# Kernel tuning notes

Measured on AMD Instinct MI355X. Metric: run time of the kernel, lower is better.

The kernel has to match this reference:

```python
import jax, jax.numpy as jnp
import numpy as np
from functools import partial

BLUR_K = 5
SIGMA = 1.5
DOWN = 4
SCALE = 5.0
OFFSET = 0.2

_DN = ('NCHW', 'OIHW', 'NCHW')


def _gaussian_kernel(k, sigma):
    x = jnp.arange(k, dtype=jnp.float32) - (k - 1) / 2.0
    g = jnp.exp(-x ** 2 / (2.0 * sigma ** 2))
    g2 = jnp.outer(g, g)
    g2 = g2 / g2.sum()
    return g2.reshape(1, 1, k, k)


def setup_inputs() -> dict:
    key = jax.random.key(0)
    left_rgb = jax.random.uniform(key, (16, 3, 544, 960), dtype=jnp.float32)
    return {"left_rgb": left_rgb}


def reference(left_rgb):
    B, C, H, W = left_rgb.shape
    # rgb -> gray (1x1 conv with fixed weights)
    w = jnp.array([0.2989, 0.587, 0.114], dtype=left_rgb.dtype)
    gray = jnp.einsum('bchw,c->bhw', left_rgb, w)[:, None]  # [B,1,H,W]

    # gaussian blur with reflect padding (torch F.pad mode='reflect')
    pad = BLUR_K // 2
    gray_p = jnp.pad(gray, ((0, 0), (0, 0), (pad, pad), (pad, pad)), mode='reflect')
    gk = _gaussian_kernel(BLUR_K, SIGMA).astype(left_rgb.dtype)
    gray_smooth = jax.lax.conv_general_dilated(gray_p, gk, (1, 1), 'VALID',
                                               dimension_numbers=_DN)

    # sobel gradients (cross-correlation, zero padding=1, same as torch conv2d)
    sx = jnp.array([[-1., 0., 1.], [-2., 0., 2.], [-1., 0., 1.]],
                   dtype=left_rgb.dtype).reshape(1, 1, 3, 3)
    sy = jnp.array([[-1., -2., -1.], [0., 0., 0.], [1., 2., 1.]],
                   dtype=left_rgb.dtype).reshape(1, 1, 3, 3)
    gx = jax.lax.conv_general_dilated(gray_smooth, sx, (1, 1), [(1, 1), (1, 1)],
                                      dimension_numbers=_DN)
    gy = jax.lax.conv_general_dilated(gray_smooth, sy, (1, 1), [(1, 1), (1, 1)],
                                      dimension_numbers=_DN)
    mag = jnp.sqrt(gx ** 2 + gy ** 2 + 1e-6)  # [B,1,H,W]

    # avg_pool2d kernel=stride=DOWN (H, W divisible by DOWN)
    down = mag.reshape(B, 1, H // DOWN, DOWN, W // DOWN, DOWN).mean(axis=(3, 5))

    edge_mask = jax.nn.sigmoid(SCALE * (down - OFFSET)) ** 2.0
    return edge_mask
```

## Files before the change

kernel.cpp:

```cpp
#include <hip/hip_runtime.h>
#include <cmath>

constexpr int B = 16, C = 3, H = 544, W = 960;
constexpr int OH = 136, OW = 240;
constexpr size_t HW = (size_t)H * W;

constexpr int TOH = 8, TOW = 30, NTH = 17, NTW = 8, MH = 32, MW = 120;
constexpr int TR = 40;
constexpr int TS = 132;
constexpr int TC4 = 32;
constexpr int NT = 5;

__global__ __launch_bounds__(256)
void edge_fused(const float* __restrict__ in, float* __restrict__ out,
                float gn0, float gn1, float gn2)
{
    __shared__ float tmp[TR * TS];

    const int tid = threadIdx.x;
    const int blk = blockIdx.x;
    const int tw = blk % NTW;
    const int th = (blk / NTW) % NTH;
    const int b  = blk / (NTW * NTH);
    const int mh0 = th * MH, mw0 = tw * MW;
    const float* inb = in + (size_t)b * C * HW;

    float4 Aq[NT][3], Bq[NT][3];
    float  Sc[NT][3];
    #pragma unroll
    for (int k = 0; k < NT; ++k) {
        const int idx = tid + 256 * k;
        const int r = idx >> 5;
        const int c = idx & 31;
        int g = mh0 - 4 + r;
        g = g < 0 ? -g : (g >= H ? 2 * H - 2 - g : g);
        int gcb = mw0 - 4 + 4 * c;
        gcb = gcb < 0 ? 0 : (gcb > W - 12 ? W - 12 : gcb);
        const float* p = inb + (size_t)g * W + gcb;
        #pragma unroll
        for (int ch = 0; ch < 3; ++ch) {
            Aq[k][ch] = *reinterpret_cast<const float4*>(p);
            Bq[k][ch] = *reinterpret_cast<const float4*>(p + 4);
            Sc[k][ch] = p[8];
            p += HW;
        }
    }
    #pragma unroll
    for (int k = 0; k < NT; ++k) {
        const int idx = tid + 256 * k;
        const int r = idx >> 5;
        const int c = idx & 31;
        const float a0[8] = {Aq[k][0].y, Aq[k][0].z, Aq[k][0].w, Bq[k][0].x,
                             Bq[k][0].y, Bq[k][0].z, Bq[k][0].w, Sc[k][0]};
        const float a1[8] = {Aq[k][1].y, Aq[k][1].z, Aq[k][1].w, Bq[k][1].x,
                             Bq[k][1].y, Bq[k][1].z, Bq[k][1].w, Sc[k][1]};
        const float a2[8] = {Aq[k][2].y, Aq[k][2].z, Aq[k][2].w, Bq[k][2].x,
                             Bq[k][2].y, Bq[k][2].z, Bq[k][2].w, Sc[k][2]};
        float g8[8];
        #pragma unroll
        for (int m = 0; m < 8; ++m)
            g8[m] = fmaf(0.2989f, a0[m], fmaf(0.587f, a1[m], 0.114f * a2[m]));
        float4 t;
        t.x = gn0 * g8[0] + gn1 * g8[1] + gn2 * g8[2] + gn1 * g8[3] + gn0 * g8[4];
        t.y = gn0 * g8[1] + gn1 * g8[2] + gn2 * g8[3] + gn1 * g8[4] + gn0 * g8[5];
        t.z = gn0 * g8[2] + gn1 * g8[3] + gn2 * g8[4] + gn1 * g8[5] + gn0 * g8[6];
        t.w = gn0 * g8[3] + gn1 * g8[4] + gn2 * g8[5] + gn1 * g8[6] + gn0 * g8[7];
        *reinterpret_cast<float4*>(&tmp[r * TS + 4 * c]) = t;
    }
    __syncthreads();

    if (tw == 0 || tw == NTW - 1) {
        const int ntask = (tw == 0) ? TR : 2 * TR;
        if (tid < ntask) {
            int r, c;
            if (tw == 0) { r = tid; c = 0; }
            else         { r = tid >> 1; c = 29 + (tid & 1); }
            int g = mh0 - 4 + r;
            g = g < 0 ? -g : (g >= H ? 2 * H - 2 - g : g);
            const int gcb = mw0 - 4 + 4 * c;
            float g8[8];
            #pragma unroll
            for (int m = 0; m < 8; ++m) {
                int gc = gcb + 1 + m;
                gc = gc < 0 ? -gc : (gc >= W ? 2 * W - 2 - gc : gc);
                const float* p = inb + (size_t)g * W + gc;
                g8[m] = 0.2989f * p[0] + 0.587f * p[HW] + 0.114f * p[2 * HW];
            }
            float4 t;
            t.x = gn0 * g8[0] + gn1 * g8[1] + gn2 * g8[2] + gn1 * g8[3] + gn0 * g8[4];
            t.y = gn0 * g8[1] + gn1 * g8[2] + gn2 * g8[3] + gn1 * g8[4] + gn0 * g8[5];
            t.z = gn0 * g8[2] + gn1 * g8[3] + gn2 * g8[4] + gn1 * g8[5] + gn0 * g8[6];
            t.w = gn0 * g8[3] + gn1 * g8[4] + gn2 * g8[5] + gn1 * g8[6] + gn0 * g8[7];
            *reinterpret_cast<float4*>(&tmp[r * TS + 4 * c]) = t;
        }
    }
    __syncthreads();

    if (tid < TOH * TOW) {
        const int orow = tid / TOW;
        const int ocol = tid - orow * TOW;
        const int sr0 = orow * 4, tc0 = ocol * 4;

        float sm[6][6];
        #pragma unroll
        for (int i = 0; i < 6; ++i)
            #pragma unroll
            for (int j = 0; j < 6; ++j) sm[i][j] = 0.f;

        const float gk[5] = {gn0, gn1, gn2, gn1, gn0};
        #pragma unroll
        for (int tr = 0; tr < 10; ++tr) {
            const float* p = &tmp[(sr0 + 1 + tr) * TS + tc0];
            const float4 u  = *reinterpret_cast<const float4*>(p);
            const float4 vv = *reinterpret_cast<const float4*>(p + 4);
            const float t6[6] = {u.x, u.y, u.z, u.w, vv.x, vv.y};
            #pragma unroll
            for (int i = 0; i < 6; ++i) {
                const int k = tr - i;
                if (k >= 0 && k < 5) {
                    #pragma unroll
                    for (int j = 0; j < 6; ++j)
                        sm[i][j] = fmaf(gk[k], t6[j], sm[i][j]);
                }
            }
        }

        #pragma unroll
        for (int i = 0; i < 6; ++i) {
            const int hh = mh0 - 1 + sr0 + i;
            const float rm = (hh >= 0 && hh < H) ? 1.f : 0.f;
            #pragma unroll
            for (int j = 0; j < 6; ++j) {
                const int ww = mw0 - 1 + tc0 + j;
                sm[i][j] *= rm * ((ww >= 0 && ww < W) ? 1.f : 0.f);
            }
        }

        float acc[4] = {0.f, 0.f, 0.f, 0.f};
        #pragma unroll
        for (int i = 0; i < 4; ++i) {
            #pragma unroll
            for (int j = 0; j < 4; ++j) {
                const float a00 = sm[i][j],     a01 = sm[i][j + 1],     a02 = sm[i][j + 2];
                const float a10 = sm[i + 1][j],                         a12 = sm[i + 1][j + 2];
                const float a20 = sm[i + 2][j], a21 = sm[i + 2][j + 1], a22 = sm[i + 2][j + 2];
                const float gx = (a02 - a00) + 2.f * (a12 - a10) + (a22 - a20);
                const float gy = (a20 + 2.f * a21 + a22) - (a00 + 2.f * a01 + a02);
                acc[i] += sqrtf(gx * gx + gy * gy + 1e-6f);
            }
        }
        const float down = ((acc[0] + acc[1]) + (acc[2] + acc[3])) * (1.f / 16.f);
        const float x = 5.0f * (down - 0.2f);
        const float sg = 1.f / (1.f + expf(-x));
        const size_t o = ((size_t)b * OH + (th * TOH + orow)) * OW + (tw * TOW + ocol);
        out[o] = sg * sg;
    }
}

extern "C" void kernel_launch(void* const* d_in, const int* in_sizes, int n_in,
                              void* d_out, int out_size, void* d_ws, size_t ws_size,
                              hipStream_t stream) {
    const float* in = (const float*)d_in[0];
    float* out = (float*)d_out;

    const double g0 = std::exp(-4.0 / 4.5);
    const double g1 = std::exp(-1.0 / 4.5);
    const double g2 = 1.0;
    const double S = 2.0 * (g0 + g1) + g2;
    const float gn0 = (float)(g0 / S);
    const float gn1 = (float)(g1 / S);
    const float gn2 = (float)(g2 / S);

    hipLaunchKernelGGL(edge_fused, dim3(B * NTH * NTW), dim3(256), 0, stream,
                       in, out, gn0, gn1, gn2);
}
```

Before: 36.13 us.

## Store raw gray tile in shared memory and move horizontal blur to consumer

Phase 1 now loads one float4 per channel per task instead of two float4 plus a scalar, and stores plain grayscale values in shared memory. The horizontal 5-tap blur moves into the output phase, which now reads 12 columns per row and runs the vertical pass over 12 columns before applying the horizontal taps. Global load traffic and instruction count in the load phase drop, and one __syncthreads is removed. In exchange the consumer threads do more vertical FMAs (72 accumulators instead of 36), which raises register pressure.

```diff
diff --git a/kernel.cpp b/kernel.cpp
--- a/kernel.cpp
+++ b/kernel.cpp
@@ -6,16 +6,15 @@
 constexpr size_t HW = (size_t)H * W;
 
 constexpr int TOH = 8, TOW = 30, NTH = 17, NTW = 8, MH = 32, MW = 120;
-constexpr int TR = 40;
-constexpr int TS = 132;
-constexpr int TC4 = 32;
+constexpr int GR = 40;
+constexpr int GS = 132;
 constexpr int NT = 5;
 
 __global__ __launch_bounds__(256)
 void edge_fused(const float* __restrict__ in, float* __restrict__ out,
                 float gn0, float gn1, float gn2)
 {
-    __shared__ float tmp[TR * TS];
+    __shared__ float gray[GR * GS];
 
     const int tid = threadIdx.x;
     const int blk = blockIdx.x;
@@ -25,8 +24,7 @@
     const int mh0 = th * MH, mw0 = tw * MW;
     const float* inb = in + (size_t)b * C * HW;
 
-    float4 Aq[NT][3], Bq[NT][3];
-    float  Sc[NT][3];
+    float4 Rv[NT], Gv[NT], Bv[NT];
     #pragma unroll
     for (int k = 0; k < NT; ++k) {
         const int idx = tid + 256 * k;
@@ -35,104 +33,89 @@
         int g = mh0 - 4 + r;
         g = g < 0 ? -g : (g >= H ? 2 * H - 2 - g : g);
         int gcb = mw0 - 4 + 4 * c;
-        gcb = gcb < 0 ? 0 : (gcb > W - 12 ? W - 12 : gcb);
+        gcb = gcb < 0 ? 0 : (gcb > W - 4 ? W - 4 : gcb);
         const float* p = inb + (size_t)g * W + gcb;
-        #pragma unroll
-        for (int ch = 0; ch < 3; ++ch) {
-            Aq[k][ch] = *reinterpret_cast<const float4*>(p);
-            Bq[k][ch] = *reinterpret_cast<const float4*>(p + 4);
-            Sc[k][ch] = p[8];
-            p += HW;
-        }
+        Rv[k] = *reinterpret_cast<const float4*>(p);
+        Gv[k] = *reinterpret_cast<const float4*>(p + HW);
+        Bv[k] = *reinterpret_cast<const float4*>(p + 2 * HW);
     }
     #pragma unroll
     for (int k = 0; k < NT; ++k) {
         const int idx = tid + 256 * k;
         const int r = idx >> 5;
         const int c = idx & 31;
-        const float a0[8] = {Aq[k][0].y, Aq[k][0].z, Aq[k][0].w, Bq[k][0].x,
-                             Bq[k][0].y, Bq[k][0].z, Bq[k][0].w, Sc[k][0]};
-        const float a1[8] = {Aq[k][1].y, Aq[k][1].z, Aq[k][1].w, Bq[k][1].x,
-                             Bq[k][1].y, Bq[k][1].z, Bq[k][1].w, Sc[k][1]};
-        const float a2[8] = {Aq[k][2].y, Aq[k][2].z, Aq[k][2].w, Bq[k][2].x,
-                             Bq[k][2].y, Bq[k][2].z, Bq[k][2].w, Sc[k][2]};
-        float g8[8];
+        float4 g;
+        g.x = fmaf(0.2989f, Rv[k].x, fmaf(0.587f, Gv[k].x, 0.114f * Bv[k].x));
+        g.y = fmaf(0.2989f, Rv[k].y, fmaf(0.587f, Gv[k].y, 0.114f * Bv[k].y));
+        g.z = fmaf(0.2989f, Rv[k].z, fmaf(0.587f, Gv[k].z, 0.114f * Bv[k].z));
+        g.w = fmaf(0.2989f, Rv[k].w, fmaf(0.587f, Gv[k].w, 0.114f * Bv[k].w));
+        const bool edgeq = (tw == 0 && c == 0) || (tw == NTW - 1 && c == 31);
+        if (!edgeq)
+            *reinterpret_cast<float4*>(&gray[r * GS + 4 * c]) = g;
+    }
+    if ((tw == 0 || tw == NTW - 1) && tid < GR) {
+        const int r = tid;
+        const int c = (tw == 0) ? 0 : 31;
+        int g = mh0 - 4 + r;
+        g = g < 0 ? -g : (g >= H ? 2 * H - 2 - g : g);
+        float4 gv;
+        float* gp = &gv.x;
         #pragma unroll
-        for (int m = 0; m < 8; ++m)
-            g8[m] = fmaf(0.2989f, a0[m], fmaf(0.587f, a1[m], 0.114f * a2[m]));
-        float4 t;
-        t.x = gn0 * g8[0] + gn1 * g8[1] + gn2 * g8[2] + gn1 * g8[3] + gn0 * g8[4];
-        t.y = gn0 * g8[1] + gn1 * g8[2] + gn2 * g8[3] + gn1 * g8[4] + gn0 * g8[5];
-        t.z = gn0 * g8[2] + gn1 * g8[3] + gn2 * g8[4] + gn1 * g8[5] + gn0 * g8[6];
-        t.w = gn0 * g8[3] + gn1 * g8[4] + gn2 * g8[5] + gn1 * g8[6] + gn0 * g8[7];
-        *reinterpret_cast<float4*>(&tmp[r * TS + 4 * c]) = t;
-    }
-    __syncthreads();
-
-    if (tw == 0 || tw == NTW - 1) {
-        const int ntask = (tw == 0) ? TR : 2 * TR;
-        if (tid < ntask) {
-            int r, c;
-            if (tw == 0) { r = tid; c = 0; }
-            else         { r = tid >> 1; c = 29 + (tid & 1); }
-            int g = mh0 - 4 + r;
-            g = g < 0 ? -g : (g >= H ? 2 * H - 2 - g : g);
-            const int gcb = mw0 - 4 + 4 * c;
-            float g8[8];
-            #pragma unroll
-            for (int m = 0; m < 8; ++m) {
-                int gc = gcb + 1 + m;
-                gc = gc < 0 ? -gc : (gc >= W ? 2 * W - 2 - gc : gc);
-                const float* p = inb + (size_t)g * W + gc;
-                g8[m] = 0.2989f * p[0] + 0.587f * p[HW] + 0.114f * p[2 * HW];
-            }
-            float4 t;
-            t.x = gn0 * g8[0] + gn1 * g8[1] + gn2 * g8[2] + gn1 * g8[3] + gn0 * g8[4];
-            t.y = gn0 * g8[1] + gn1 * g8[2] + gn2 * g8[3] + gn1 * g8[4] + gn0 * g8[5];
-            t.z = gn0 * g8[2] + gn1 * g8[3] + gn2 * g8[4] + gn1 * g8[5] + gn0 * g8[6];
-            t.w = gn0 * g8[3] + gn1 * g8[4] + gn2 * g8[5] + gn1 * g8[6] + gn0 * g8[7];
-            *reinterpret_cast<float4*>(&tmp[r * TS + 4 * c]) = t;
+        for (int m = 0; m < 4; ++m) {
+            int gc = mw0 - 4 + 4 * c + m;
+            gc = gc < 0 ? -gc : (gc >= W ? 2 * W - 2 - gc : gc);
+            const float* p = inb + (size_t)g * W + gc;
+            gp[m] = 0.2989f * p[0] + 0.587f * p[HW] + 0.114f * p[2 * HW];
         }
+        *reinterpret_cast<float4*>(&gray[r * GS + 4 * c]) = gv;
     }
     __syncthreads();
 
     if (tid < TOH * TOW) {
         const int orow = tid / TOW;
         const int ocol = tid - orow * TOW;
-        const int sr0 = orow * 4, tc0 = ocol * 4;
+        const int lc0 = 4 * ocol;
+        const int rb = 4 * orow + 1;
 
-        float sm[6][6];
+        float vb[6][12];
         #pragma unroll
         for (int i = 0; i < 6; ++i)
             #pragma unroll
-            for (int j = 0; j < 6; ++j) sm[i][j] = 0.f;
+            for (int j = 0; j < 12; ++j) vb[i][j] = 0.f;
 
         const float gk[5] = {gn0, gn1, gn2, gn1, gn0};
         #pragma unroll
         for (int tr = 0; tr < 10; ++tr) {
-            const float* p = &tmp[(sr0 + 1 + tr) * TS + tc0];
-            const float4 u  = *reinterpret_cast<const float4*>(p);
-            const float4 vv = *reinterpret_cast<const float4*>(p + 4);
-            const float t6[6] = {u.x, u.y, u.z, u.w, vv.x, vv.y};
+            const float* p = &gray[(rb + tr) * GS + lc0];
+            const float4 u = *reinterpret_cast<const float4*>(p);
+            const float4 v = *reinterpret_cast<const float4*>(p + 4);
+            const float4 w = *reinterpret_cast<const float4*>(p + 8);
+            const float t12[12] = {u.x, u.y, u.z, u.w, v.x, v.y, v.z, v.w,
+                                   w.x, w.y, w.z, w.w};
             #pragma unroll
             for (int i = 0; i < 6; ++i) {
-                const int k = tr - i;
-                if (k >= 0 && k < 5) {
+                const int m = tr - i;
+                if (m >= 0 && m < 5) {
                     #pragma unroll
-                    for (int j = 0; j < 6; ++j)
-                        sm[i][j] = fmaf(gk[k], t6[j], sm[i][j]);
+                    for (int j = 0; j < 12; ++j)
+                        vb[i][j] = fmaf(gk[m], t12[j], vb[i][j]);
                 }
             }
         }
 
+        float sm6[6][6];
         #pragma unroll
         for (int i = 0; i < 6; ++i) {
-            const int hh = mh0 - 1 + sr0 + i;
+            const int hh = mh0 + 4 * orow - 1 + i;
             const float rm = (hh >= 0 && hh < H) ? 1.f : 0.f;
             #pragma unroll
             for (int j = 0; j < 6; ++j) {
-                const int ww = mw0 - 1 + tc0 + j;
-                sm[i][j] *= rm * ((ww >= 0 && ww < W) ? 1.f : 0.f);
+                const float s5 = fmaf(gn0, vb[i][1 + j] + vb[i][5 + j],
+                                 fmaf(gn1, vb[i][2 + j] + vb[i][4 + j],
+                                      gn2 * vb[i][3 + j]));
+                const int ww = mw0 + 4 * ocol - 1 + j;
+                const float cm = (ww >= 0 && ww < W) ? 1.f : 0.f;
+                sm6[i][j] = s5 * rm * cm;
             }
         }
 
@@ -141,9 +124,9 @@
         for (int i = 0; i < 4; ++i) {
             #pragma unroll
             for (int j = 0; j < 4; ++j) {
-                const float a00 = sm[i][j],     a01 = sm[i][j + 1],     a02 = sm[i][j + 2];
-                const float a10 = sm[i + 1][j],                         a12 = sm[i + 1][j + 2];
-                const float a20 = sm[i + 2][j], a21 = sm[i + 2][j + 1], a22 = sm[i + 2][j + 2];
+                const float a00 = sm6[i][j],     a01 = sm6[i][j + 1],     a02 = sm6[i][j + 2];
+                const float a10 = sm6[i + 1][j],                          a12 = sm6[i + 1][j + 2];
+                const float a20 = sm6[i + 2][j], a21 = sm6[i + 2][j + 1], a22 = sm6[i + 2][j + 2];
                 const float gx = (a02 - a00) + 2.f * (a12 - a10) + (a22 - a20);
                 const float gy = (a20 + 2.f * a21 + a22) - (a00 + 2.f * a01 + a02);
                 acc[i] += sqrtf(gx * gx + gy * gy + 1e-6f);
```

After: 33.98 us. -5.9%, faster.
